# Optimization experiments

Hardware: AMD Instinct MI355X
Metric: run time of the kernel (lower is better)

The kernel has to match this reference:

```python
import jax, jax.numpy as jnp
import numpy as np

N = 50000      # nodes
E = 800000     # edges
F = 500        # num_features
HID = 64       # hidden_channels
H = 4          # num_heads
HC = HID // H  # headc = 16
C = 8          # num_classes
KHOP = 2       # K hops
CST = 1e-5


def setup_inputs() -> dict:
    key = jax.random.key(0)
    ks = jax.random.split(key, 12)
    s = 0.02
    return {
        "node_feat": jax.random.normal(ks[0], (N, F), dtype=jnp.float32),
        "edge_index": jax.random.randint(ks[1], (2, E), 0, N, dtype=jnp.int64),
        "Wi": jax.random.normal(ks[2], (F, HID), dtype=jnp.float32) * s,
        "bi": jnp.zeros((HID,), dtype=jnp.float32),
        "Wq": jax.random.normal(ks[3], (HID, H * HC), dtype=jnp.float32) * s,
        "bq": jnp.zeros((H * HC,), dtype=jnp.float32),
        "Wk": jax.random.normal(ks[4], (HID, H * HC), dtype=jnp.float32) * s,
        "bk": jnp.zeros((H * HC,), dtype=jnp.float32),
        "Wv": jax.random.normal(ks[5], (HID, H * C), dtype=jnp.float32) * s,
        "bv": jnp.zeros((H * C,), dtype=jnp.float32),
        "Wo": jax.random.normal(ks[6], (H * C, C), dtype=jnp.float32) * s,
        "bo": jnp.zeros((C,), dtype=jnp.float32),
        "hopwise": jnp.ones((KHOP + 1,), dtype=jnp.float32),
        "headwise": jnp.zeros((H, KHOP), dtype=jnp.float32),
        "teleport": jnp.ones((1,), dtype=jnp.float32),
    }


def reference(node_feat, edge_index, Wi, bi, Wq, bq, Wk, bk, Wv, bv, Wo, bo,
              hopwise, headwise, teleport):
    row, col = edge_index[0], edge_index[1]
    # degree(col): in-degree; norm = deg^-1 indexed at row (as in the torch code)
    deg = jax.ops.segment_sum(jnp.ones((E,), dtype=node_feat.dtype), col,
                              num_segments=N)
    deg_inv = jnp.where(deg > 0, 1.0 / deg, 0.0)  # [N]

    x = jax.nn.relu(node_feat @ Wi + bi)          # dropout p=0.0 / eval -> identity
    Q = (1.0 + jax.nn.elu(x @ Wq + bq)).reshape(N, H, HC)
    Kf = (1.0 + jax.nn.elu(x @ Wk + bk)).reshape(N, H, HC)
    V = (x @ Wv + bv).reshape(N, H, C)

    M = jnp.einsum('nhi,nhj->nhij', Kf, V)        # [N,H,HC,C]
    hidden = V * hopwise[0]                       # ind_gamma & gamma_softmax
    layerwise = jax.nn.softmax(headwise, axis=0)  # softmax over heads (dim=-2)

    # global attention (teleport) term
    teleportM = jnp.sum(M, axis=0, keepdims=True) / N      # [1,H,HC,C]
    teleportK = jnp.sum(Kf, axis=0, keepdims=True) / N     # [1,H,HC]
    teleportH = jnp.einsum('nhi,bhij->nhj', Q, teleportM)  # [N,H,C]
    teleportC = jnp.einsum('nhi,bhi->nh', Q, teleportK)[..., None] + CST
    teleportH = (teleportH / teleportC).sum(axis=-2)       # [N,C]

    for hop in range(KHOP):
        # norm[e] = deg_inv[row[e]]  =>  pre-scale source nodes, then scatter-add
        M = jax.ops.segment_sum((M * deg_inv[:, None, None, None])[row], col,
                                num_segments=N)
        Kf = jax.ops.segment_sum((Kf * deg_inv[:, None, None])[row], col,
                                 num_segments=N)
        Hh = jnp.einsum('nhi,nhij->nhj', Q, M)             # [N,H,C]
        Cc = jnp.einsum('nhi,nhi->nh', Q, Kf)[..., None] + CST
        gamma = hopwise[hop + 1] * layerwise[:, hop][:, None]  # [H,1]
        hidden = hidden + gamma * (Hh / Cc)

    # multi_concat output projection
    hidden = hidden.reshape(N, H * C) @ Wo + bo
    return hidden + teleport * teleportH
```

## Files before the change

### kernel.cpp

```cpp
#include <hip/hip_runtime.h>
#include <hip/hip_bf16.h>
#include <stdint.h>
#include <stddef.h>

#define NN 50000
#define NE 800000
#define FIN 500
#define HIDN 64
#define NH 4
#define HCD 16
#define NC 8
#define KVROW 192
#define SROW 576
#define CSTF 1e-5f
#define SCAN_NB 196
#define NTILES 782

typedef float f32x2 __attribute__((ext_vector_type(2)));
typedef __attribute__((ext_vector_type(8))) short bf16x8;
typedef __attribute__((ext_vector_type(4))) float f32x4;

__device__ inline float bf_lo(unsigned u) {
    union { unsigned i; float f; } v; v.i = u << 16; return v.f;
}
__device__ inline f32x2 bfpair(unsigned u) {
    union { unsigned i; float f; } lo, hi;
    lo.i = u << 16; hi.i = u & 0xffff0000u;
    f32x2 r; r.x = lo.f; r.y = hi.f; return r;
}
__device__ inline unsigned short f2bf(float f) {
    union { float f; unsigned i; } v; v.f = f;
    unsigned r = v.i + 0x7fffu + ((v.i >> 16) & 1u);
    return (unsigned short)(r >> 16);
}
__device__ inline unsigned pack2bf(float a, float b) {
    __hip_bfloat162 h = __float22bfloat162_rn(make_float2(a, b));
    unsigned r; __builtin_memcpy(&r, &h, 4); return r;
}


__global__ void k_deg_wt(const int* __restrict__ col, int* __restrict__ deg,
                         const float* __restrict__ Wi, unsigned short* __restrict__ Wt) {
    int e = blockIdx.x * blockDim.x + threadIdx.x;
    if (e < NE) atomicAdd(&deg[col[e]], 1);
    if (e < 64 * 512) {
        int c = e >> 9;
        int k = e & 511;
        Wt[e] = (k < FIN) ? f2bf(Wi[(size_t)k * 64 + c]) : (unsigned short)0;
    }
}


__global__ void k_bsum(const int* __restrict__ deg, int* __restrict__ bsum,
                       float* __restrict__ dinv, int* __restrict__ cursor,
                       float* __restrict__ tMK) {
    __shared__ int red[256];
    int b = blockIdx.x, t = threadIdx.x;
    int i = b * 256 + t;
    int d = (i < NN) ? deg[i] : 0;
    if (i < NN) {
        dinv[i] = d > 0 ? 1.0f / (float)d : 0.0f;
        cursor[i] = 0;
    }
    if (b == 0)
        for (int j = t; j < 576; j += 256) tMK[j] = 0.f;
    red[t] = d;
    __syncthreads();
    for (int s = 128; s > 0; s >>= 1) {
        if (t < s) red[t] += red[t + s];
        __syncthreads();
    }
    if (t == 0) bsum[b] = red[0];
}

__global__ void k_bscan(const int* __restrict__ bsum, int* __restrict__ bex) {
    __shared__ int s[256];
    int t = threadIdx.x;
    int own = (t < SCAN_NB) ? bsum[t] : 0;
    s[t] = own;
    __syncthreads();
    for (int d = 1; d < 256; d <<= 1) {
        int v = (t >= d) ? s[t - d] : 0;
        __syncthreads();
        s[t] += v;
        __syncthreads();
    }
    if (t < SCAN_NB) bex[t] = s[t] - own;
}

__global__ void k_expand(const int* __restrict__ deg, const int* __restrict__ bex,
                         int* __restrict__ offs) {
    __shared__ int s[256];
    int b = blockIdx.x, t = threadIdx.x;
    int i = b * 256 + t;
    int v = (i < NN) ? deg[i] : 0;
    s[t] = v;
    __syncthreads();
    for (int d = 1; d < 256; d <<= 1) {
        int a = (t >= d) ? s[t - d] : 0;
        __syncthreads();
        s[t] += a;
        __syncthreads();
    }
    int excl = s[t] - v + bex[b];
    if (i < NN) offs[i] = excl;
    if (i == NN - 1) offs[NN] = excl + v;
}

__global__ void k_scatter(const int* __restrict__ row, const int* __restrict__ col,
                          const int* __restrict__ offs, int* __restrict__ cursor,
                          int* __restrict__ csr_src) {
    int e = blockIdx.x * blockDim.x + threadIdx.x;
    if (e < NE) {
        int c = col[e];
        int pos = offs[c] + atomicAdd(&cursor[c], 1);
        csr_src[pos] = row[e];
    }
}


__global__ __launch_bounds__(256) void k_xgemm(const float* __restrict__ nf,
                                               const unsigned short* __restrict__ Wt,
                                               const float* __restrict__ bi,
                                               float* __restrict__ x) {
    int t = threadIdx.x;
    int lane = t & 63;
    int w = t >> 6;
    int quad = lane >> 4;
    int l15 = lane & 15;
    int n0 = blockIdx.x * 64;
    int rown = n0 + w * 16 + l15;
    const float* arow = &nf[(size_t)(rown < NN ? rown : 0) * FIN];

    f32x4 acc[4];
#pragma unroll
    for (int ct = 0; ct < 4; ct++) acc[ct] = (f32x4){0.f, 0.f, 0.f, 0.f};

    for (int k0 = 0; k0 < 512; k0 += 32) {
        int kk = k0 + quad * 8;
        float4 a0 = make_float4(0.f, 0.f, 0.f, 0.f);
        float4 a1 = make_float4(0.f, 0.f, 0.f, 0.f);
        if (kk < FIN) a0 = *(const float4*)&arow[kk];
        if (kk + 4 < FIN) a1 = *(const float4*)&arow[kk + 4];
        union { unsigned u[4]; bf16x8 v; } A;
        A.u[0] = pack2bf(a0.x, a0.y);
        A.u[1] = pack2bf(a0.z, a0.w);
        A.u[2] = pack2bf(a1.x, a1.y);
        A.u[3] = pack2bf(a1.z, a1.w);
#pragma unroll
        for (int ct = 0; ct < 4; ct++) {
            int c = ct * 16 + l15;
            bf16x8 bfr = *(const bf16x8*)&Wt[(size_t)c * 512 + kk];
            acc[ct] = __builtin_amdgcn_mfma_f32_16x16x32_bf16(A.v, bfr, acc[ct], 0, 0, 0);
        }
    }
#pragma unroll
    for (int ct = 0; ct < 4; ct++) {
        int c = ct * 16 + l15;
        float bv = bi[c];
#pragma unroll
        for (int r = 0; r < 4; r++) {
            int n = n0 + w * 16 + quad * 4 + r;
            if (n < NN)
                x[(size_t)n * 64 + c] = fmaxf(acc[ct][r] + bv, 0.f);
        }
    }
}


__global__ __launch_bounds__(256) void k_qkv(const float* __restrict__ x,
    const float* __restrict__ Wq, const float* __restrict__ bq,
    const float* __restrict__ Wk, const float* __restrict__ bk,
    const float* __restrict__ Wv, const float* __restrict__ bv,
    const float* __restrict__ hopwise, const float* __restrict__ dinv,
    float* __restrict__ Qg, float* __restrict__ hid,
    unsigned char* __restrict__ kv0, float* __restrict__ tMK) {
    __shared__ float wq_s[64 * 64], wk_s[64 * 64], wv_s[64 * 32];
    __shared__ float bq_s[64], bk_s[64], bv_s[32];
    __shared__ float xs[4][8][64];
    __shared__ float tacc[576];
    int t = threadIdx.x;
    for (int i = t; i < 4096; i += 256) { wq_s[i] = Wq[i]; wk_s[i] = Wk[i]; }
    for (int i = t; i < 2048; i += 256) wv_s[i] = Wv[i];
    if (t < 64) { bq_s[t] = bq[t]; bk_s[t] = bk[t]; }
    if (t >= 64 && t < 96) bv_s[t - 64] = bv[t - 64];
    for (int i = t; i < 576; i += 256) tacc[i] = 0.f;
    __syncthreads();
    int lane = t & 63;
    int w = t >> 6;
    int h = lane >> 4;
    int vcol = lane & 31;
    float hw0 = hopwise[0];
    float tkp = 0.f;
    float tmp_[8];
#pragma unroll
    for (int j = 0; j < 8; j++) tmp_[j] = 0.f;
    int tiles = (NN + 31) >> 5;
    for (int tile = blockIdx.x; tile < tiles; tile += gridDim.x) {
        int n0 = tile * 32 + w * 8;
        __syncthreads();
#pragma unroll
        for (int u = 0; u < 8; u++) {
            int n = n0 + u;
            xs[w][u][lane] = (n < NN) ? x[(size_t)n * 64 + lane] : 0.f;
        }
        __syncthreads();
        float aq[8], ak[8], av[8];
#pragma unroll
        for (int u = 0; u < 8; u++) { aq[u] = 0.f; ak[u] = 0.f; av[u] = 0.f; }
        for (int f = 0; f < 64; f++) {
            float wqv = wq_s[f * 64 + lane];
            float wkv = wk_s[f * 64 + lane];
            float wvv = wv_s[f * 32 + vcol];
#pragma unroll
            for (int u = 0; u < 8; u++) {
                float xf = xs[w][u][f];
                aq[u] = fmaf(xf, wqv, aq[u]);
                ak[u] = fmaf(xf, wkv, ak[u]);
                av[u] = fmaf(xf, wvv, av[u]);
            }
        }
#pragma unroll
        for (int u = 0; u < 8; u++) {
            int n = n0 + u;
            float q = aq[u] + bq_s[lane];
            float k = ak[u] + bk_s[lane];
            float v = av[u] + bv_s[vcol];
            float Qv = q > 0.f ? 1.f + q : expf(q);
            float Kv = k > 0.f ? 1.f + k : expf(k);
            if (n < NN) {
                Qg[(size_t)n * 64 + lane] = Qv;
                float vj[8];
#pragma unroll
                for (int j = 0; j < 8; j++) vj[j] = __shfl(v, h * 8 + j, 64);
                tkp += Kv;
#pragma unroll
                for (int j = 0; j < 8; j++) tmp_[j] += Kv * vj[j];
                float dv = dinv[n];
                unsigned short* kvrow = (unsigned short*)(kv0 + (size_t)n * KVROW);
                kvrow[lane] = f2bf(Kv * dv);
                if (lane < 32) kvrow[64 + lane] = f2bf(v);
                if (lane < 32) hid[(size_t)n * 32 + lane] = v * hw0;
            }
        }
    }
#pragma unroll
    for (int j = 0; j < 8; j++) atomicAdd(&tacc[lane * 8 + j], tmp_[j]);
    atomicAdd(&tacc[512 + lane], tkp);
    __syncthreads();
    for (int i = t; i < 576; i += 256) atomicAdd(&tMK[i], tacc[i]);
}


__global__ __launch_bounds__(256) void k_hop0(const unsigned char* __restrict__ kv0,
    const int* __restrict__ offs, const int* __restrict__ csr_src,
    const float* __restrict__ dinv, const float* __restrict__ Qg,
    const float* __restrict__ hopwise, const float* __restrict__ headwise,
    unsigned char* __restrict__ S1, float* __restrict__ hid) {
    int t = threadIdx.x;
    int lane = t & 63;
    int n = __builtin_amdgcn_readfirstlane((blockIdx.x * 256 + t) >> 6);
    if (n >= NN) return;
    int h = lane >> 4;
    float e0 = expf(headwise[0]);
    float e1 = expf(headwise[2]);
    float e2 = expf(headwise[4]);
    float e3 = expf(headwise[6]);
    float esum = e0 + e1 + e2 + e3;
    float eh = (h == 0) ? e0 : ((h == 1) ? e1 : ((h == 2) ? e2 : e3));
    float gam = hopwise[1] * eh / esum;

    int hoff = 128 + h * 16;
    int o0 = offs[n], o1 = offs[n + 1];
    float kacc = 0.f;
    f32x2 A0 = {0.f, 0.f}, A1 = {0.f, 0.f}, B0 = {0.f, 0.f}, B1 = {0.f, 0.f};
    int e = o0;
    for (; e + 7 < o1; e += 8) {
        float kk_[8]; uint4 vv[8];
#pragma unroll
        for (int q = 0; q < 8; q++) {
            int s = csr_src[e + q];
            const unsigned char* r = kv0 + (size_t)s * KVROW;
            kk_[q] = bf_lo(((const unsigned short*)r)[lane]);
            vv[q] = *(const uint4*)(r + hoff);
        }
#pragma unroll
        for (int q = 0; q < 8; q++) {
            float ka = kk_[q];
            f32x2 ka2; ka2.x = ka; ka2.y = ka;
            kacc += ka;
            A0 += ka2 * bfpair(vv[q].x);
            A1 += ka2 * bfpair(vv[q].y);
            B0 += ka2 * bfpair(vv[q].z);
            B1 += ka2 * bfpair(vv[q].w);
        }
    }
    for (; e < o1; e++) {
        int s = csr_src[e];
        const unsigned char* r = kv0 + (size_t)s * KVROW;
        float ka = bf_lo(((const unsigned short*)r)[lane]);
        uint4 va = *(const uint4*)(r + hoff);
        f32x2 ka2; ka2.x = ka; ka2.y = ka;
        kacc += ka;
        A0 += ka2 * bfpair(va.x);
        A1 += ka2 * bfpair(va.y);
        B0 += ka2 * bfpair(va.z);
        B1 += ka2 * bfpair(va.w);
    }
    {
        float dv = dinv[n];
        float s8 = dv * 8.f;
        float s16 = dv * 16.f;
        unsigned char* drow = S1 + (size_t)n * SROW;
        unsigned kb8 = __builtin_amdgcn_cvt_pk_fp8_f32(kacc * s8, 0.f, 0, false);
        drow[lane] = (unsigned char)(kb8 & 0xff);
        unsigned u0 = __builtin_amdgcn_cvt_pk_fp8_f32(A0.x * s16, A0.y * s16, 0, false);
        u0 = __builtin_amdgcn_cvt_pk_fp8_f32(A1.x * s16, A1.y * s16, u0, true);
        unsigned u1 = __builtin_amdgcn_cvt_pk_fp8_f32(B0.x * s16, B0.y * s16, 0, false);
        u1 = __builtin_amdgcn_cvt_pk_fp8_f32(B1.x * s16, B1.y * s16, u1, true);
        uint2 pv; pv.x = u0; pv.y = u1;
        *(uint2*)(drow + 64 + lane * 8) = pv;
    }
    float qv = Qg[(size_t)n * 64 + lane];
    float hh[8];
    hh[0] = qv * A0.x; hh[1] = qv * A0.y; hh[2] = qv * A1.x; hh[3] = qv * A1.y;
    hh[4] = qv * B0.x; hh[5] = qv * B0.y; hh[6] = qv * B1.x; hh[7] = qv * B1.y;
    float cc = qv * kacc;
#pragma unroll
    for (int s = 1; s < 16; s <<= 1) {
#pragma unroll
        for (int j = 0; j < 8; j++) hh[j] += __shfl_xor(hh[j], s, 16);
        cc += __shfl_xor(cc, s, 16);
    }
    if ((lane & 15) < 8) {
        int j = lane & 7;
        float val = j < 4 ? (j < 2 ? (j == 0 ? hh[0] : hh[1]) : (j == 2 ? hh[2] : hh[3]))
                          : (j < 6 ? (j == 4 ? hh[4] : hh[5]) : (j == 6 ? hh[6] : hh[7]));
        size_t idx = (size_t)n * 32 + h * 8 + j;
        hid[idx] += gam * val / (cc + CSTF);
    }
}


__global__ __launch_bounds__(256) void k_prop1(const unsigned char* __restrict__ Sold,
    const int* __restrict__ offs, const int* __restrict__ csr_src,
    const float* __restrict__ Qg, const float* __restrict__ hopwise,
    const float* __restrict__ headwise, float* __restrict__ hid) {
    int t = threadIdx.x;
    int lane = t & 63;
    int n = __builtin_amdgcn_readfirstlane((blockIdx.x * 256 + t) >> 6);
    if (n >= NN) return;
    int h = lane >> 4;
    float e0 = expf(headwise[1]);
    float e1 = expf(headwise[3]);
    float e2 = expf(headwise[5]);
    float e3 = expf(headwise[7]);
    float esum = e0 + e1 + e2 + e3;
    float eh = (h == 0) ? e0 : ((h == 1) ? e1 : ((h == 2) ? e2 : e3));
    float gam = hopwise[2] * eh / esum * 0.0625f;

    int o0 = offs[n], o1 = offs[n + 1];
    float kacc = 0.f;
    f32x2 A0 = {0.f, 0.f}, A1 = {0.f, 0.f}, B0 = {0.f, 0.f}, B1 = {0.f, 0.f};
    int e = o0;
    for (; e + 7 < o1; e += 8) {
        unsigned kb[8]; uint2 mv[8];
#pragma unroll
        for (int q = 0; q < 8; q++) {
            int s = csr_src[e + q];
            const unsigned char* r = Sold + (size_t)s * SROW;
            kb[q] = r[lane];
            mv[q] = *(const uint2*)(r + 64 + lane * 8);
        }
#pragma unroll
        for (int q = 0; q < 8; q++) {
            f32x2 kv = __builtin_amdgcn_cvt_pk_f32_fp8(kb[q], false);
            kacc += kv.x;
            A0 += __builtin_amdgcn_cvt_pk_f32_fp8(mv[q].x, false);
            A1 += __builtin_amdgcn_cvt_pk_f32_fp8(mv[q].x, true);
            B0 += __builtin_amdgcn_cvt_pk_f32_fp8(mv[q].y, false);
            B1 += __builtin_amdgcn_cvt_pk_f32_fp8(mv[q].y, true);
        }
    }
    for (; e < o1; e++) {
        int s = csr_src[e];
        const unsigned char* r = Sold + (size_t)s * SROW;
        unsigned kb = r[lane];
        uint2 mva = *(const uint2*)(r + 64 + lane * 8);
        f32x2 kv = __builtin_amdgcn_cvt_pk_f32_fp8(kb, false);
        kacc += kv.x;
        A0 += __builtin_amdgcn_cvt_pk_f32_fp8(mva.x, false);
        A1 += __builtin_amdgcn_cvt_pk_f32_fp8(mva.x, true);
        B0 += __builtin_amdgcn_cvt_pk_f32_fp8(mva.y, false);
        B1 += __builtin_amdgcn_cvt_pk_f32_fp8(mva.y, true);
    }
    kacc *= 0.125f;
    float qv = Qg[(size_t)n * 64 + lane];
    float hh[8];
    hh[0] = qv * A0.x; hh[1] = qv * A0.y; hh[2] = qv * A1.x; hh[3] = qv * A1.y;
    hh[4] = qv * B0.x; hh[5] = qv * B0.y; hh[6] = qv * B1.x; hh[7] = qv * B1.y;
    float cc = qv * kacc;
#pragma unroll
    for (int s = 1; s < 16; s <<= 1) {
#pragma unroll
        for (int j = 0; j < 8; j++) hh[j] += __shfl_xor(hh[j], s, 16);
        cc += __shfl_xor(cc, s, 16);
    }
    if ((lane & 15) < 8) {
        int j = lane & 7;
        float val = j < 4 ? (j < 2 ? (j == 0 ? hh[0] : hh[1]) : (j == 2 ? hh[2] : hh[3]))
                          : (j < 6 ? (j == 4 ? hh[4] : hh[5]) : (j == 6 ? hh[6] : hh[7]));
        size_t idx = (size_t)n * 32 + h * 8 + j;
        hid[idx] += gam * val / (cc + CSTF);
    }
}


__global__ __launch_bounds__(256) void k_final(const float* __restrict__ hid,
    const float* __restrict__ Qg, const float* __restrict__ Wo,
    const float* __restrict__ bo, const float* __restrict__ tMK,
    const float* __restrict__ teleport, float* __restrict__ out) {
    __shared__ float tm[512];
    __shared__ float tk[64];
    __shared__ float wo[256];
    __shared__ float bos[8];
    int t = threadIdx.x;
    const float invN = 1.0f / (float)NN;
    for (int i = t; i < 512; i += 256) tm[i] = tMK[i] * invN;
    if (t < 64) tk[t] = tMK[512 + t] * invN;
    wo[t] = Wo[t & 255];
    if (t < 8) bos[t] = bo[t];
    __syncthreads();
    float tp = teleport[0];
    int lane = t & 63;
    int sub = lane & 7;
    int g = lane >> 3;
    int wid = (blockIdx.x * 256 + t) >> 6;
    int nwaves = gridDim.x * 4;
    for (int nb = wid * 8; nb < NN; nb += nwaves * 8) {
        int n = nb + g;
        if (n < NN) {
            const float* hrow = hid + (size_t)n * 32;
            const float* qrow = Qg + (size_t)n * 64;
            float o = bos[sub];
#pragma unroll
            for (int m = 0; m < 32; m++) o = fmaf(hrow[m], wo[m * 8 + sub], o);
            float th = 0.f;
#pragma unroll
            for (int h2 = 0; h2 < 4; h2++) {
                float num = 0.f, den = 0.f;
#pragma unroll
                for (int i = 0; i < 16; i++) {
                    float q = qrow[h2 * 16 + i];
                    num = fmaf(q, tm[h2 * 128 + i * 8 + sub], num);
                    den = fmaf(q, tk[h2 * 16 + i], den);
                }
                th += num / (den + CSTF);
            }
            out[(size_t)n * 8 + sub] = o + tp * th;
        }
    }
}


extern "C" void kernel_launch(void* const* d_in, const int* in_sizes, int n_in,
                              void* d_out, int out_size, void* d_ws, size_t ws_size,
                              hipStream_t stream) {
    const float* nf = (const float*)d_in[0];
    const int* ei = (const int*)d_in[1];
    const float* Wi = (const float*)d_in[2];
    const float* bi = (const float*)d_in[3];
    const float* Wq = (const float*)d_in[4];
    const float* bq = (const float*)d_in[5];
    const float* Wk = (const float*)d_in[6];
    const float* bk = (const float*)d_in[7];
    const float* Wv = (const float*)d_in[8];
    const float* bv = (const float*)d_in[9];
    const float* Wo = (const float*)d_in[10];
    const float* bo = (const float*)d_in[11];
    const float* hopwise = (const float*)d_in[12];
    const float* headwise = (const float*)d_in[13];
    const float* teleport = (const float*)d_in[14];
    float* out = (float*)d_out;

    char* base = (char*)d_ws;
    size_t off = 0;
    auto alloc = [&](size_t bytes) -> void* {
        void* p = base + off;
        off = (off + bytes + 255) & ~(size_t)255;
        return p;
    };
    int* deg = (int*)alloc(NN * 4);
    int* cursor = (int*)alloc(NN * 4);
    int* offs = (int*)alloc((NN + 1) * 4);
    int* bsum = (int*)alloc(256 * 4);
    int* bex = (int*)alloc(256 * 4);
    float* dinv = (float*)alloc(NN * 4);
    int* csr_src = (int*)alloc((size_t)NE * 4);
    unsigned short* Wt = (unsigned short*)alloc(64 * 512 * 2);
    float* xbuf = (float*)alloc((size_t)NN * 64 * 4);
    float* Qg = (float*)alloc((size_t)NN * 64 * 4);
    float* hid = (float*)alloc((size_t)NN * 32 * 4);
    unsigned char* kv0 = (unsigned char*)alloc((size_t)NN * KVROW);
    unsigned char* S1 = (unsigned char*)alloc((size_t)NN * SROW);
    float* tMK = (float*)alloc(576 * 4);

    const int* rowp = ei;
    const int* colp = ei + NE;

    hipMemsetAsync(deg, 0, NN * 4, stream);

    k_deg_wt<<<(NE + 255) / 256, 256, 0, stream>>>(colp, deg, Wi, Wt);
    k_bsum<<<SCAN_NB, 256, 0, stream>>>(deg, bsum, dinv, cursor, tMK);
    k_bscan<<<1, 256, 0, stream>>>(bsum, bex);
    k_expand<<<SCAN_NB, 256, 0, stream>>>(deg, bex, offs);
    k_scatter<<<(NE + 255) / 256, 256, 0, stream>>>(rowp, colp, offs, cursor, csr_src);
    k_xgemm<<<NTILES, 256, 0, stream>>>(nf, Wt, bi, xbuf);
    k_qkv<<<768, 256, 0, stream>>>(xbuf, Wq, bq, Wk, bk, Wv, bv, hopwise, dinv,
                                   Qg, hid, kv0, tMK);
    k_hop0<<<(NN * 64 + 255) / 256, 256, 0, stream>>>(kv0, offs, csr_src, dinv, Qg,
                                                      hopwise, headwise, S1, hid);
    k_prop1<<<(NN * 64 + 255) / 256, 256, 0, stream>>>(S1, offs, csr_src, Qg,
                                                       hopwise, headwise, hid);
    k_final<<<1563, 256, 0, stream>>>(hid, Qg, Wo, bo, tMK, teleport, out);
}
```

Before: 462.7 us.

## Stage node-feature tile through double-buffered swizzled LDS with coalesced prefetch in xgemm

Rewrites the input-projection GEMM so that each block cooperatively loads a 64x64 slab of node features with coalesced float4 reads. The slab is converted to bf16 and stored in an XOR-swizzled LDS tile, with double buffering so the next slab's global loads overlap the current slab's MFMAs. This replaces the strided per-lane row reads from global memory. It adds LDS use, a barrier per k-step, and more register pressure from the prefetch buffers.

After: 469.2 us. Within noise of the previous version (+1.4%).

```diff
diff --git a/kernel.cpp b/kernel.cpp
--- a/kernel.cpp
+++ b/kernel.cpp
@@ -123,37 +123,85 @@
                                                const unsigned short* __restrict__ Wt,
                                                const float* __restrict__ bi,
                                                float* __restrict__ x) {
+    __shared__ __align__(16) unsigned short atile[2][64 * 64];
     int t = threadIdx.x;
     int lane = t & 63;
     int w = t >> 6;
     int quad = lane >> 4;
     int l15 = lane & 15;
     int n0 = blockIdx.x * 64;
-    int rown = n0 + w * 16 + l15;
-    const float* arow = &nf[(size_t)(rown < NN ? rown : 0) * FIN];
+
+    int srow = t >> 2;
+    int sseg = t & 3;
+    int srg = n0 + srow;
+    if (srg >= NN) srg = NN - 1;
+    const float* sp = nf + (size_t)srg * FIN + sseg * 16;
+    unsigned ssw = (unsigned)((srow & 7) << 4);
+    unsigned wb0 = (unsigned)(srow * 128) + (((unsigned)(sseg * 32)) ^ ssw);
+    unsigned wb1 = (unsigned)(srow * 128) + (((unsigned)(sseg * 32 + 16)) ^ ssw);
+
+    int rowl = w * 16 + l15;
+    unsigned csw = (unsigned)((rowl & 7) << 4);
+    unsigned rb0 = (unsigned)(rowl * 128) + (((unsigned)(quad * 16)) ^ csw);
+    unsigned rb1 = (unsigned)(rowl * 128) + (((unsigned)(64 + quad * 16)) ^ csw);
 
     f32x4 acc[4];
 #pragma unroll
     for (int ct = 0; ct < 4; ct++) acc[ct] = (f32x4){0.f, 0.f, 0.f, 0.f};
 
-    for (int k0 = 0; k0 < 512; k0 += 32) {
-        int kk = k0 + quad * 8;
-        float4 a0 = make_float4(0.f, 0.f, 0.f, 0.f);
-        float4 a1 = make_float4(0.f, 0.f, 0.f, 0.f);
-        if (kk < FIN) a0 = *(const float4*)&arow[kk];
-        if (kk + 4 < FIN) a1 = *(const float4*)&arow[kk + 4];
-        union { unsigned u[4]; bf16x8 v; } A;
-        A.u[0] = pack2bf(a0.x, a0.y);
-        A.u[1] = pack2bf(a0.z, a0.w);
-        A.u[2] = pack2bf(a1.x, a1.y);
-        A.u[3] = pack2bf(a1.z, a1.w);
-#pragma unroll
-        for (int ct = 0; ct < 4; ct++) {
-            int c = ct * 16 + l15;
-            bf16x8 bfr = *(const bf16x8*)&Wt[(size_t)c * 512 + kk];
-            acc[ct] = __builtin_amdgcn_mfma_f32_16x16x32_bf16(A.v, bfr, acc[ct], 0, 0, 0);
-        }
-    }
+    float4 vcur[4];
+#pragma unroll
+    for (int j = 0; j < 4; ++j) vcur[j] = *(const float4*)(sp + j * 4);
+    {
+        union { unsigned u[4]; bf16x8 b; } p0, p1;
+        p0.u[0] = pack2bf(vcur[0].x, vcur[0].y); p0.u[1] = pack2bf(vcur[0].z, vcur[0].w);
+        p0.u[2] = pack2bf(vcur[1].x, vcur[1].y); p0.u[3] = pack2bf(vcur[1].z, vcur[1].w);
+        p1.u[0] = pack2bf(vcur[2].x, vcur[2].y); p1.u[1] = pack2bf(vcur[2].z, vcur[2].w);
+        p1.u[2] = pack2bf(vcur[3].x, vcur[3].y); p1.u[3] = pack2bf(vcur[3].z, vcur[3].w);
+        *(bf16x8*)((char*)atile[0] + wb0) = p0.b;
+        *(bf16x8*)((char*)atile[0] + wb1) = p1.b;
+    }
+    __syncthreads();
+
+#pragma unroll
+    for (int ks = 0; ks < 8; ks++) {
+        float4 vn[4];
+        if (ks < 7) {
+            int k0n = (ks + 1) * 64;
+#pragma unroll
+            for (int j = 0; j < 4; ++j) {
+                int kk = k0n + sseg * 16 + j * 4;
+                if (kk < FIN) vn[j] = *(const float4*)(sp + k0n + j * 4);
+                else vn[j] = make_float4(0.f, 0.f, 0.f, 0.f);
+            }
+        }
+        {
+            const char* buf = (const char*)atile[ks & 1];
+            bf16x8 a0 = *(const bf16x8*)(buf + rb0);
+            bf16x8 a1 = *(const bf16x8*)(buf + rb1);
+            int kk0 = ks * 64 + quad * 8;
+#pragma unroll
+            for (int ct = 0; ct < 4; ct++) {
+                const unsigned short* wp = &Wt[(size_t)(ct * 16 + l15) * 512];
+                bf16x8 b0 = *(const bf16x8*)&wp[kk0];
+                bf16x8 b1 = *(const bf16x8*)&wp[kk0 + 32];
+                acc[ct] = __builtin_amdgcn_mfma_f32_16x16x32_bf16(a0, b0, acc[ct], 0, 0, 0);
+                acc[ct] = __builtin_amdgcn_mfma_f32_16x16x32_bf16(a1, b1, acc[ct], 0, 0, 0);
+            }
+        }
+        if (ks < 7) {
+            union { unsigned u[4]; bf16x8 b; } p0, p1;
+            p0.u[0] = pack2bf(vn[0].x, vn[0].y); p0.u[1] = pack2bf(vn[0].z, vn[0].w);
+            p0.u[2] = pack2bf(vn[1].x, vn[1].y); p0.u[3] = pack2bf(vn[1].z, vn[1].w);
+            p1.u[0] = pack2bf(vn[2].x, vn[2].y); p1.u[1] = pack2bf(vn[2].z, vn[2].w);
+            p1.u[2] = pack2bf(vn[3].x, vn[3].y); p1.u[3] = pack2bf(vn[3].z, vn[3].w);
+            char* nbuf = (char*)atile[(ks + 1) & 1];
+            *(bf16x8*)(nbuf + wb0) = p0.b;
+            *(bf16x8*)(nbuf + wb1) = p1.b;
+            __syncthreads();
+        }
+    }
+
 #pragma unroll
     for (int ct = 0; ct < 4; ct++) {
         int c = ct * 16 + l15;
```

## Stage node_feat tile in swizzled LDS with coalesced row loads for input GEMM

Applied to the files above, without the earlier changes.

The input projection GEMM now has each wave load 16 full node-feature rows with coalesced float4 loads. It converts them to bf16 and stores them in a 64KB XOR-swizzled shared-memory tile, then reads MFMA A-fragments from LDS. Before this, each lane read strided 32-byte chunks straight from global memory, so accesses were poorly coalesced. The cost is 64KB of LDS per block, which lowers occupancy, and many registers held for the preloaded rows.

Result: no change. 467.3 us (+1.0%).

```diff
diff --git a/kernel.cpp b/kernel.cpp
--- a/kernel.cpp
+++ b/kernel.cpp
@@ -123,37 +123,59 @@
                                                const unsigned short* __restrict__ Wt,
                                                const float* __restrict__ bi,
                                                float* __restrict__ x) {
+    __shared__ __align__(16) unsigned short atile[64 * 512];
     int t = threadIdx.x;
     int lane = t & 63;
     int w = t >> 6;
     int quad = lane >> 4;
     int l15 = lane & 15;
     int n0 = blockIdx.x * 64;
-    int rown = n0 + w * 16 + l15;
-    const float* arow = &nf[(size_t)(rown < NN ? rown : 0) * FIN];
+
+    float4 va[16], vb[16];
+#pragma unroll
+    for (int i = 0; i < 16; i++) {
+        int rg = n0 + w * 16 + i;
+        if (rg >= NN) rg = NN - 1;
+        const float* rp = nf + (size_t)rg * FIN;
+        va[i] = *(const float4*)(rp + 4 * lane);
+        vb[i] = (lane <= 60) ? *(const float4*)(rp + 256 + 4 * lane)
+                             : make_float4(0.f, 0.f, 0.f, 0.f);
+    }
+#pragma unroll
+    for (int i = 0; i < 16; i++) {
+        int r = w * 16 + i;
+        char* rowp = (char*)atile + r * 1024;
+        unsigned sw = (unsigned)((r & 7) << 4);
+        uint2 p0, p1;
+        p0.x = pack2bf(va[i].x, va[i].y); p0.y = pack2bf(va[i].z, va[i].w);
+        p1.x = pack2bf(vb[i].x, vb[i].y); p1.y = pack2bf(vb[i].z, vb[i].w);
+        *(uint2*)(rowp + (((unsigned)(8 * lane)) ^ sw)) = p0;
+        *(uint2*)(rowp + (((unsigned)(512 + 8 * lane)) ^ sw)) = p1;
+    }
+
+    int rowl = w * 16 + l15;
+    const char* arow = (const char*)atile + rowl * 1024;
+    unsigned swc = (unsigned)((rowl & 7) << 4);
 
     f32x4 acc[4];
 #pragma unroll
     for (int ct = 0; ct < 4; ct++) acc[ct] = (f32x4){0.f, 0.f, 0.f, 0.f};
 
-    for (int k0 = 0; k0 < 512; k0 += 32) {
-        int kk = k0 + quad * 8;
-        float4 a0 = make_float4(0.f, 0.f, 0.f, 0.f);
-        float4 a1 = make_float4(0.f, 0.f, 0.f, 0.f);
-        if (kk < FIN) a0 = *(const float4*)&arow[kk];
-        if (kk + 4 < FIN) a1 = *(const float4*)&arow[kk + 4];
-        union { unsigned u[4]; bf16x8 v; } A;
-        A.u[0] = pack2bf(a0.x, a0.y);
-        A.u[1] = pack2bf(a0.z, a0.w);
-        A.u[2] = pack2bf(a1.x, a1.y);
-        A.u[3] = pack2bf(a1.z, a1.w);
+#pragma unroll
+    for (int ks = 0; ks < 8; ks++) {
+        bf16x8 a0 = *(const bf16x8*)(arow + (((unsigned)(ks * 128 + quad * 16)) ^ swc));
+        bf16x8 a1 = *(const bf16x8*)(arow + (((unsigned)(ks * 128 + quad * 16 + 64)) ^ swc));
+        int kk0 = ks * 64 + quad * 8;
 #pragma unroll
         for (int ct = 0; ct < 4; ct++) {
-            int c = ct * 16 + l15;
-            bf16x8 bfr = *(const bf16x8*)&Wt[(size_t)c * 512 + kk];
-            acc[ct] = __builtin_amdgcn_mfma_f32_16x16x32_bf16(A.v, bfr, acc[ct], 0, 0, 0);
-        }
-    }
+            const unsigned short* wp = &Wt[(size_t)(ct * 16 + l15) * 512];
+            bf16x8 b0 = *(const bf16x8*)&wp[kk0];
+            bf16x8 b1 = *(const bf16x8*)&wp[kk0 + 32];
+            acc[ct] = __builtin_amdgcn_mfma_f32_16x16x32_bf16(a0, b0, acc[ct], 0, 0, 0);
+            acc[ct] = __builtin_amdgcn_mfma_f32_16x16x32_bf16(a1, b1, acc[ct], 0, 0, 0);
+        }
+    }
+
 #pragma unroll
     for (int ct = 0; ct < 4; ct++) {
         int c = ct * 16 + l15;
```

## Split-K the input projection GEMM across waves with LDS reduction

Applied to the files above, without the earlier changes.

The input-projection GEMM is restructured so each block handles 16 rows instead of 64. Its four waves each cover a quarter of the K dimension, with all A-row loads issued up front, and the partial MFMA sums are reduced through shared memory before the bias and ReLU. This raises the block count and the number of loads in flight, to better hide the latency of streaming the large feature matrix. The cost is an extra LDS round-trip and a barrier per block. Reads past the 500-column edge are clamped rather than zeroed, which assumes the padded weight columns are zero.

New measurement: 455.5 us. About the same (-1.6%).

```diff
diff --git a/kernel.cpp b/kernel.cpp
--- a/kernel.cpp
+++ b/kernel.cpp
@@ -14,7 +14,7 @@
 #define SROW 576
 #define CSTF 1e-5f
 #define SCAN_NB 196
-#define NTILES 782
+#define XBLKS 3125
 
 typedef float f32x2 __attribute__((ext_vector_type(2)));
 typedef __attribute__((ext_vector_type(8))) short bf16x8;
@@ -123,47 +123,61 @@
                                                const unsigned short* __restrict__ Wt,
                                                const float* __restrict__ bi,
                                                float* __restrict__ x) {
+    __shared__ float red[4][16][68];
     int t = threadIdx.x;
     int lane = t & 63;
     int w = t >> 6;
     int quad = lane >> 4;
     int l15 = lane & 15;
-    int n0 = blockIdx.x * 64;
-    int rown = n0 + w * 16 + l15;
-    const float* arow = &nf[(size_t)(rown < NN ? rown : 0) * FIN];
+    int n0 = blockIdx.x * 16;
+    const float* rp = nf + (size_t)(n0 + l15) * FIN;
+    int kbase = w * 128;
+
+    float4 a0[4], a1[4];
+#pragma unroll
+    for (int ks = 0; ks < 4; ks++) {
+        int kk = kbase + ks * 32 + quad * 8;
+        int c0 = kk > 496 ? 496 : kk;
+        int c1 = kk + 4 > 496 ? 496 : kk + 4;
+        a0[ks] = *(const float4*)(rp + c0);
+        a1[ks] = *(const float4*)(rp + c1);
+    }
 
     f32x4 acc[4];
 #pragma unroll
     for (int ct = 0; ct < 4; ct++) acc[ct] = (f32x4){0.f, 0.f, 0.f, 0.f};
 
-    for (int k0 = 0; k0 < 512; k0 += 32) {
-        int kk = k0 + quad * 8;
-        float4 a0 = make_float4(0.f, 0.f, 0.f, 0.f);
-        float4 a1 = make_float4(0.f, 0.f, 0.f, 0.f);
-        if (kk < FIN) a0 = *(const float4*)&arow[kk];
-        if (kk + 4 < FIN) a1 = *(const float4*)&arow[kk + 4];
+#pragma unroll
+    for (int ks = 0; ks < 4; ks++) {
         union { unsigned u[4]; bf16x8 v; } A;
-        A.u[0] = pack2bf(a0.x, a0.y);
-        A.u[1] = pack2bf(a0.z, a0.w);
-        A.u[2] = pack2bf(a1.x, a1.y);
-        A.u[3] = pack2bf(a1.z, a1.w);
+        A.u[0] = pack2bf(a0[ks].x, a0[ks].y);
+        A.u[1] = pack2bf(a0[ks].z, a0[ks].w);
+        A.u[2] = pack2bf(a1[ks].x, a1[ks].y);
+        A.u[3] = pack2bf(a1[ks].z, a1[ks].w);
+        int kk = kbase + ks * 32 + quad * 8;
 #pragma unroll
         for (int ct = 0; ct < 4; ct++) {
-            int c = ct * 16 + l15;
-            bf16x8 bfr = *(const bf16x8*)&Wt[(size_t)c * 512 + kk];
-            acc[ct] = __builtin_amdgcn_mfma_f32_16x16x32_bf16(A.v, bfr, acc[ct], 0, 0, 0);
-        }
-    }
-#pragma unroll
-    for (int ct = 0; ct < 4; ct++) {
-        int c = ct * 16 + l15;
-        float bv = bi[c];
-#pragma unroll
-        for (int r = 0; r < 4; r++) {
-            int n = n0 + w * 16 + quad * 4 + r;
-            if (n < NN)
-                x[(size_t)n * 64 + c] = fmaxf(acc[ct][r] + bv, 0.f);
-        }
+            bf16x8 b = *(const bf16x8*)&Wt[(size_t)(ct * 16 + l15) * 512 + kk];
+            acc[ct] = __builtin_amdgcn_mfma_f32_16x16x32_bf16(A.v, b, acc[ct], 0, 0, 0);
+        }
+    }
+
+#pragma unroll
+    for (int ct = 0; ct < 4; ct++)
+#pragma unroll
+        for (int r = 0; r < 4; r++)
+            red[w][quad * 4 + r][ct * 16 + l15] = acc[ct][r];
+    __syncthreads();
+
+    int ocol = t & 63;
+    int orow0 = t >> 6;
+    float bv = bi[ocol];
+#pragma unroll
+    for (int i = 0; i < 4; i++) {
+        int orow = i * 4 + orow0;
+        float s = red[0][orow][ocol] + red[1][orow][ocol]
+                + red[2][orow][ocol] + red[3][orow][ocol];
+        x[(size_t)(n0 + orow) * 64 + ocol] = fmaxf(s + bv, 0.f);
     }
 }
 
@@ -515,7 +529,7 @@
     k_bscan<<<1, 256, 0, stream>>>(bsum, bex);
     k_expand<<<SCAN_NB, 256, 0, stream>>>(deg, bex, offs);
     k_scatter<<<(NE + 255) / 256, 256, 0, stream>>>(rowp, colp, offs, cursor, csr_src);
-    k_xgemm<<<NTILES, 256, 0, stream>>>(nf, Wt, bi, xbuf);
+    k_xgemm<<<XBLKS, 256, 0, stream>>>(nf, Wt, bi, xbuf);
     k_qkv<<<768, 256, 0, stream>>>(xbuf, Wq, bq, Wk, bk, Wv, bv, hopwise, dinv,
                                    Qg, hid, kv0, tMK);
     k_hop0<<<(NN * 64 + 255) / 256, 256, 0, stream>>>(kv0, offs, csr_src, dinv, Qg,
```
